# Optimization experiments

Hardware: AMD Instinct MI355X
Metric: run time of the kernel (lower is better)

## Reference

```python
import jax, jax.numpy as jnp
import numpy as np

B, C, H = 128, 3, 224
PATCH_NUM, PS = 14, 16          # patch_size = image_size / patch_num
NP = PATCH_NUM * PATCH_NUM      # 196 patches
TOP_K = 20
D = 768                         # ViT-B hidden dim
NUM_CLASSES = 1000


def setup_inputs() -> dict:
    key = jax.random.key(0)
    k1, k2, k3, k4, k5 = jax.random.split(key, 5)
    return {
        "inputs": jax.random.normal(k1, (B, C, H, H), jnp.float32),
        "patch_grad": jax.random.normal(k2, (B, NP, D), jnp.float32),
        "attack_w": jax.random.uniform(k3, (C, H, H), jnp.float32),  # torch.rand init
        "w_cls": jax.random.normal(k4, (C * NP, NUM_CLASSES), jnp.float32) * 0.02,
        "targets": jax.random.randint(k5, (B,), 0, NUM_CLASSES),
    }


def reference(inputs, patch_grad, attack_w, w_cls, targets):
    # --- top-k patch selection from patch-embedding gradients ---
    # sum over batch, then over embedding dim -> [NP]
    sum_patch = patch_grad.sum(axis=0).sum(axis=1)
    _, top_idx = jax.lax.top_k(sum_patch, TOP_K)  # distinct patch indices

    # --- vectorized equivalent of the per-pixel double loop ---
    # patch (ix, iy) -> pixel block [ix*PS:(ix+1)*PS, iy*PS:(iy+1)*PS]
    ix = top_idx // PATCH_NUM
    iy = top_idx % PATCH_NUM
    mask_p = jnp.zeros((PATCH_NUM, PATCH_NUM), inputs.dtype).at[ix, iy].set(1.0)
    mask = jnp.kron(mask_p, jnp.ones((PS, PS), inputs.dtype))  # [H, H] pixel mask
    x = inputs + mask[None, None, :, :] * attack_w[None, :, :, :]  # [B,C,H,H]

    # --- surrogate classifier head (stand-in for aux_vit second forward) ---
    # per-patch average pool, flatten, linear -> logits [B, NUM_CLASSES]
    pooled = x.reshape(B, C, PATCH_NUM, PS, PATCH_NUM, PS).mean(axis=(3, 5))
    logits = pooled.reshape(B, -1) @ w_cls

    targets_prob = jax.nn.softmax(logits, axis=1)
    # original applies CrossEntropyLoss to the *probabilities* (treats them as logits)
    logp = jax.nn.log_softmax(targets_prob, axis=1)
    ce = -jnp.take_along_axis(logp, targets[:, None], axis=1)[:, 0]  # [B]

    u = 0.0
    l2loss = jnp.mean(attack_w * attack_w)
    loss = u * l2loss - (1.0 - u) * ce.mean()
    return targets_prob, loss
```

## Files before the change

kernel.cpp:

```cpp
#include <hip/hip_runtime.h>
#include <math.h>

#define PA_OFF    0
#define APOOL_OFF 1024
#define MA_OFF    2048
#define IPOOL_OFF 4096
#define PL_OFF    81920

__global__ __launch_bounds__(256) void k1_fused(
    const float* __restrict__ inputs,
    const float* __restrict__ patch_grad,
    const float* __restrict__ attack_w,
    float* __restrict__ ws)
{
  __shared__ __align__(16) float lds[3136];
  const int bid = blockIdx.x;
  const int t   = threadIdx.x;

  if (bid < 384) {
    const int b = bid / 3, c = bid - b * 3;
    const float* img = inputs + (size_t)bid * 50176;
    if (t < 224) {
      const int c4 = t % 56, rg = t / 56;
      for (int px = 0; px < 14; ++px) {
        float s = 0.f;
        #pragma unroll
        for (int jj = 0; jj < 4; ++jj) {
          const int row = px * 16 + jj * 4 + rg;
          const float4 v = *(const float4*)(img + row * 224 + c4 * 4);
          s += v.x + v.y + v.z + v.w;
        }
        lds[(px * 4 + rg) * 56 + c4] = s;
      }
    }
    __syncthreads();
    if (t < 196) {
      const int px = t / 14, py = t - px * 14;
      float s = 0.f;
      #pragma unroll
      for (int rg = 0; rg < 4; ++rg)
        #pragma unroll
        for (int i4 = 0; i4 < 4; ++i4)
          s += lds[(px * 4 + rg) * 56 + py * 4 + i4];
      ws[IPOOL_OFF + (size_t)b * 588 + c * 196 + t] = s * (1.f / 256.f);
    }
  } else if (bid < 1168) {
    const int a = bid - 384;
    const int p = a >> 2, chunk = a & 3;
    const float* base = patch_grad + (size_t)chunk * 32 * 150528 + (size_t)p * 768;
    float ax = 0, ay = 0, az = 0, aw = 0;
    #pragma unroll
    for (int j = 0; j < 24; ++j) {
      const int idx = j * 256 + t;
      const int r   = idx / 192;
      const int off = idx - r * 192;
      const float4 v = *(const float4*)(base + (size_t)r * 150528 + off * 4);
      ax += v.x; ay += v.y; az += v.z; aw += v.w;
    }
    float acc = (ax + ay) + (az + aw);
    #pragma unroll
    for (int o = 32; o > 0; o >>= 1) acc += __shfl_down(acc, o, 64);
    if ((t & 63) == 0) lds[t >> 6] = acc;
    __syncthreads();
    if (t == 0) ws[PA_OFF + a] = lds[0] + lds[1] + lds[2] + lds[3];
  } else {
    const int a = bid - 1168;
    const int c = a / 14, px = a - c * 14;
    const float* img = attack_w + (size_t)c * 50176;
    if (t < 224) {
      const int c4 = t % 56, rg = t / 56;
      float s = 0.f;
      #pragma unroll
      for (int jj = 0; jj < 4; ++jj) {
        const int row = px * 16 + jj * 4 + rg;
        const float4 v = *(const float4*)(img + row * 224 + c4 * 4);
        s += v.x + v.y + v.z + v.w;
      }
      lds[rg * 56 + c4] = s;
    }
    __syncthreads();
    if (t < 14) {
      float s = 0.f;
      #pragma unroll
      for (int rg = 0; rg < 4; ++rg)
        for (int i4 = 0; i4 < 4; ++i4)
          s += lds[rg * 56 + t * 4 + i4];
      ws[APOOL_OFF + c * 196 + px * 14 + t] = s * (1.f / 256.f);
    }
  }
}

__global__ __launch_bounds__(256) void k2_topk(float* __restrict__ ws,
                                               float* __restrict__ d_loss)
{
  __shared__ float sp[196];
  __shared__ float maskp[196];
  const int t = threadIdx.x;
  if (t < 196) {
    const float* pa = ws + PA_OFF;
    float s = 0.f;
    #pragma unroll
    for (int j = 0; j < 4; ++j) s += pa[t * 4 + j];
    sp[t] = s;
  }
  if (t == 0) *d_loss = 0.f;
  __syncthreads();
  if (t < 196) {
    const float v = sp[t];
    int cnt = 0;
    for (int j = 0; j < 196; ++j) {
      const float u = sp[j];
      cnt += (u > v || (u == v && j < t)) ? 1 : 0;
    }
    maskp[t] = (cnt < 20) ? 1.f : 0.f;
  }
  __syncthreads();
  for (int k = t; k < 588; k += 256) {
    const int p = k % 196;
    ws[MA_OFF + k] = maskp[p] * ws[APOOL_OFF + k];
  }
}

__global__ __launch_bounds__(256) void k3_gemm(const float* __restrict__ w_cls,
                                               float* __restrict__ ws)
{
  __shared__ __align__(16) float lp[147 * 16];
  const int bid = blockIdx.x;
  const int ks = bid & 3;
  const int nt = (bid >> 2) & 15;
  const int bg = bid >> 6;
  const int t  = threadIdx.x;
  const float* ipool = ws + IPOOL_OFF;
  const float* ma    = ws + MA_OFF;
  for (int idx = t; idx < 2352; idx += 256) {
    const int bb = idx / 147;
    const int kk = idx - bb * 147;
    const int k  = ks * 147 + kk;
    lp[kk * 16 + bb] = ipool[(size_t)(bg * 16 + bb) * 588 + k] + ma[k];
  }
  __syncthreads();
  const int lane = t & 63, g = t >> 6;
  const int n = nt * 64 + lane;
  const bool valid = n < 1000;
  float a0 = 0, a1 = 0, a2 = 0, a3 = 0;
  const float* wc = w_cls + (size_t)ks * 147 * 1000 + n;
  #pragma unroll 7
  for (int kk = 0; kk < 147; ++kk) {
    const float w = valid ? wc[(size_t)kk * 1000] : 0.f;
    const float4 pv = *(const float4*)&lp[kk * 16 + g * 4];
    a0 += pv.x * w; a1 += pv.y * w; a2 += pv.z * w; a3 += pv.w * w;
  }
  float* pl = ws + PL_OFF;
  const int rowb = ks * 128 + bg * 16 + g * 4;
  pl[(size_t)(rowb + 0) * 1024 + n] = a0;
  pl[(size_t)(rowb + 1) * 1024 + n] = a1;
  pl[(size_t)(rowb + 2) * 1024 + n] = a2;
  pl[(size_t)(rowb + 3) * 1024 + n] = a3;
}

__global__ __launch_bounds__(256) void k4_softmax(const float* __restrict__ ws,
                                                  const int* __restrict__ targets,
                                                  float* __restrict__ out)
{
  __shared__ float red[4];
  __shared__ float sh_pt;
  const int b = blockIdx.x, t = threadIdx.x;
  const float* pl = ws + PL_OFF;
  float l[4]; bool val[4];
  #pragma unroll
  for (int j = 0; j < 4; ++j) {
    const int n = j * 256 + t;
    val[j] = (n < 1000);
    float s = -INFINITY;
    if (val[j]) {
      s = 0.f;
      #pragma unroll
      for (int ks = 0; ks < 4; ++ks) s += pl[(size_t)(ks * 128 + b) * 1024 + n];
    }
    l[j] = s;
  }
  float m = fmaxf(fmaxf(l[0], l[1]), fmaxf(l[2], l[3]));
  #pragma unroll
  for (int o = 32; o > 0; o >>= 1) m = fmaxf(m, __shfl_down(m, o, 64));
  if ((t & 63) == 0) red[t >> 6] = m;
  __syncthreads();
  const float m1 = fmaxf(fmaxf(red[0], red[1]), fmaxf(red[2], red[3]));
  __syncthreads();
  float e[4]; float s = 0.f;
  #pragma unroll
  for (int j = 0; j < 4; ++j) { e[j] = val[j] ? expf(l[j] - m1) : 0.f; s += e[j]; }
  #pragma unroll
  for (int o = 32; o > 0; o >>= 1) s += __shfl_down(s, o, 64);
  if ((t & 63) == 0) red[t >> 6] = s;
  __syncthreads();
  const float S1 = red[0] + red[1] + red[2] + red[3];
  __syncthreads();
  const float inv = 1.f / S1;
  const int tgt = targets[b];
  float p[4];
  #pragma unroll
  for (int j = 0; j < 4; ++j) {
    const int n = j * 256 + t;
    if (val[j]) {
      p[j] = e[j] * inv;
      out[(size_t)b * 1000 + n] = p[j];
      if (n == tgt) sh_pt = p[j];
    } else {
      p[j] = -INFINITY;
    }
  }
  float m2 = fmaxf(fmaxf(p[0], p[1]), fmaxf(p[2], p[3]));
  #pragma unroll
  for (int o = 32; o > 0; o >>= 1) m2 = fmaxf(m2, __shfl_down(m2, o, 64));
  if ((t & 63) == 0) red[t >> 6] = m2;
  __syncthreads();
  const float M2 = fmaxf(fmaxf(red[0], red[1]), fmaxf(red[2], red[3]));
  __syncthreads();
  float s2 = 0.f;
  #pragma unroll
  for (int j = 0; j < 4; ++j) s2 += val[j] ? expf(p[j] - M2) : 0.f;
  #pragma unroll
  for (int o = 32; o > 0; o >>= 1) s2 += __shfl_down(s2, o, 64);
  if ((t & 63) == 0) red[t >> 6] = s2;
  __syncthreads();
  if (t == 0) {
    const float S2 = red[0] + red[1] + red[2] + red[3];
    const float lse2 = M2 + logf(S2);
    atomicAdd(out + 128000, (sh_pt - lse2) * (1.f / 128.f));
  }
}

extern "C" void kernel_launch(void* const* d_in, const int* in_sizes, int n_in,
                              void* d_out, int out_size, void* d_ws, size_t ws_size,
                              hipStream_t stream) {
  const float* inputs     = (const float*)d_in[0];
  const float* patch_grad = (const float*)d_in[1];
  const float* attack_w   = (const float*)d_in[2];
  const float* w_cls      = (const float*)d_in[3];
  const int*   targets    = (const int*)d_in[4];
  float* out = (float*)d_out;
  float* ws  = (float*)d_ws;

  hipLaunchKernelGGL(k1_fused,  dim3(1210), dim3(256), 0, stream,
                     inputs, patch_grad, attack_w, ws);
  hipLaunchKernelGGL(k2_topk,   dim3(1),    dim3(256), 0, stream, ws, out + 128000);
  hipLaunchKernelGGL(k3_gemm,   dim3(512),  dim3(256), 0, stream, w_cls, ws);
  hipLaunchKernelGGL(k4_softmax, dim3(128), dim3(256), 0, stream, ws, targets, out);
}
```

Baseline: 212.2 us.

## Split pooling, patch-grad reduction and GEMM into more, smaller blocks with batched loads

The image-pooling stage is split so each block handles two patch rows of one image channel instead of the whole image. The patch-gradient reduction uses 8 batch chunks instead of 4, and all loads are issued up front into register arrays before summing. The GEMM uses 8-batch groups per block, doubling the block count. The aim is more parallelism and more memory-level parallelism on a bandwidth-bound workload. The cost is more blocks, repeated weight reads in the GEMM, and more partials for the top-k kernel to sum.

```diff
diff --git a/kernel.cpp b/kernel.cpp
--- a/kernel.cpp
+++ b/kernel.cpp
@@ -2,8 +2,8 @@
 #include <math.h>
 
 #define PA_OFF    0
-#define APOOL_OFF 1024
-#define MA_OFF    2048
+#define APOOL_OFF 2048
+#define MA_OFF    3072
 #define IPOOL_OFF 4096
 #define PL_OFF    81920
 
@@ -13,69 +13,77 @@
     const float* __restrict__ attack_w,
     float* __restrict__ ws)
 {
-  __shared__ __align__(16) float lds[3136];
+  __shared__ __align__(16) float lds[448];
   const int bid = blockIdx.x;
   const int t   = threadIdx.x;
 
-  if (bid < 384) {
-    const int b = bid / 3, c = bid - b * 3;
-    const float* img = inputs + (size_t)bid * 50176;
+  if (bid < 2688) {
+    const int img = bid / 7, pp = bid - img * 7;
+    const float* src = inputs + (size_t)img * 50176 + (size_t)pp * 32 * 224;
     if (t < 224) {
       const int c4 = t % 56, rg = t / 56;
-      for (int px = 0; px < 14; ++px) {
-        float s = 0.f;
-        #pragma unroll
-        for (int jj = 0; jj < 4; ++jj) {
-          const int row = px * 16 + jj * 4 + rg;
-          const float4 v = *(const float4*)(img + row * 224 + c4 * 4);
-          s += v.x + v.y + v.z + v.w;
-        }
-        lds[(px * 4 + rg) * 56 + c4] = s;
+      float4 v[8];
+      #pragma unroll
+      for (int j = 0; j < 8; ++j) {
+        const int row = (j >> 2) * 16 + (j & 3) * 4 + rg;
+        v[j] = *(const float4*)(src + row * 224 + c4 * 4);
       }
+      float s0 = 0.f, s1 = 0.f;
+      #pragma unroll
+      for (int j = 0; j < 4; ++j) s0 += (v[j].x + v[j].y) + (v[j].z + v[j].w);
+      #pragma unroll
+      for (int j = 4; j < 8; ++j) s1 += (v[j].x + v[j].y) + (v[j].z + v[j].w);
+      lds[(0 * 4 + rg) * 56 + c4] = s0;
+      lds[(1 * 4 + rg) * 56 + c4] = s1;
     }
     __syncthreads();
-    if (t < 196) {
-      const int px = t / 14, py = t - px * 14;
+    if (t < 28) {
+      const int pxl = t / 14, py = t - pxl * 14;
       float s = 0.f;
       #pragma unroll
       for (int rg = 0; rg < 4; ++rg)
         #pragma unroll
         for (int i4 = 0; i4 < 4; ++i4)
-          s += lds[(px * 4 + rg) * 56 + py * 4 + i4];
-      ws[IPOOL_OFF + (size_t)b * 588 + c * 196 + t] = s * (1.f / 256.f);
-    }
-  } else if (bid < 1168) {
-    const int a = bid - 384;
-    const int p = a >> 2, chunk = a & 3;
-    const float* base = patch_grad + (size_t)chunk * 32 * 150528 + (size_t)p * 768;
-    float ax = 0, ay = 0, az = 0, aw = 0;
-    #pragma unroll
-    for (int j = 0; j < 24; ++j) {
+          s += lds[(pxl * 4 + rg) * 56 + py * 4 + i4];
+      const int b = img / 3, c = img - b * 3;
+      const int px = pp * 2 + pxl;
+      ws[IPOOL_OFF + (size_t)b * 588 + c * 196 + px * 14 + py] = s * (1.f / 256.f);
+    }
+  } else if (bid < 4256) {
+    const int a = bid - 2688;
+    const int p = a >> 3, chunk = a & 7;
+    const float* base = patch_grad + (size_t)chunk * 16 * 150528 + (size_t)p * 768;
+    float4 v[12];
+    #pragma unroll
+    for (int j = 0; j < 12; ++j) {
       const int idx = j * 256 + t;
       const int r   = idx / 192;
       const int off = idx - r * 192;
-      const float4 v = *(const float4*)(base + (size_t)r * 150528 + off * 4);
-      ax += v.x; ay += v.y; az += v.z; aw += v.w;
-    }
-    float acc = (ax + ay) + (az + aw);
+      v[j] = *(const float4*)(base + (size_t)r * 150528 + off * 4);
+    }
+    float acc = 0.f;
+    #pragma unroll
+    for (int j = 0; j < 12; ++j) acc += (v[j].x + v[j].y) + (v[j].z + v[j].w);
     #pragma unroll
     for (int o = 32; o > 0; o >>= 1) acc += __shfl_down(acc, o, 64);
     if ((t & 63) == 0) lds[t >> 6] = acc;
     __syncthreads();
     if (t == 0) ws[PA_OFF + a] = lds[0] + lds[1] + lds[2] + lds[3];
   } else {
-    const int a = bid - 1168;
+    const int a = bid - 4256;
     const int c = a / 14, px = a - c * 14;
     const float* img = attack_w + (size_t)c * 50176;
     if (t < 224) {
       const int c4 = t % 56, rg = t / 56;
-      float s = 0.f;
+      float4 v[4];
       #pragma unroll
       for (int jj = 0; jj < 4; ++jj) {
         const int row = px * 16 + jj * 4 + rg;
-        const float4 v = *(const float4*)(img + row * 224 + c4 * 4);
-        s += v.x + v.y + v.z + v.w;
+        v[jj] = *(const float4*)(img + row * 224 + c4 * 4);
       }
+      float s = 0.f;
+      #pragma unroll
+      for (int jj = 0; jj < 4; ++jj) s += (v[jj].x + v[jj].y) + (v[jj].z + v[jj].w);
       lds[rg * 56 + c4] = s;
     }
     __syncthreads();
@@ -100,7 +108,7 @@
     const float* pa = ws + PA_OFF;
     float s = 0.f;
     #pragma unroll
-    for (int j = 0; j < 4; ++j) s += pa[t * 4 + j];
+    for (int j = 0; j < 8; ++j) s += pa[t * 8 + j];
     sp[t] = s;
   }
   if (t == 0) *d_loss = 0.f;
@@ -124,7 +132,7 @@
 __global__ __launch_bounds__(256) void k3_gemm(const float* __restrict__ w_cls,
                                                float* __restrict__ ws)
 {
-  __shared__ __align__(16) float lp[147 * 16];
+  __shared__ __align__(16) float lp[147 * 8];
   const int bid = blockIdx.x;
   const int ks = bid & 3;
   const int nt = (bid >> 2) & 15;
@@ -132,30 +140,28 @@
   const int t  = threadIdx.x;
   const float* ipool = ws + IPOOL_OFF;
   const float* ma    = ws + MA_OFF;
-  for (int idx = t; idx < 2352; idx += 256) {
+  for (int idx = t; idx < 1176; idx += 256) {
     const int bb = idx / 147;
     const int kk = idx - bb * 147;
     const int k  = ks * 147 + kk;
-    lp[kk * 16 + bb] = ipool[(size_t)(bg * 16 + bb) * 588 + k] + ma[k];
+    lp[kk * 8 + bb] = ipool[(size_t)(bg * 8 + bb) * 588 + k] + ma[k];
   }
   __syncthreads();
   const int lane = t & 63, g = t >> 6;
   const int n = nt * 64 + lane;
   const bool valid = n < 1000;
-  float a0 = 0, a1 = 0, a2 = 0, a3 = 0;
+  float a0 = 0, a1 = 0;
   const float* wc = w_cls + (size_t)ks * 147 * 1000 + n;
   #pragma unroll 7
   for (int kk = 0; kk < 147; ++kk) {
     const float w = valid ? wc[(size_t)kk * 1000] : 0.f;
-    const float4 pv = *(const float4*)&lp[kk * 16 + g * 4];
-    a0 += pv.x * w; a1 += pv.y * w; a2 += pv.z * w; a3 += pv.w * w;
+    const float2 pv = *(const float2*)&lp[kk * 8 + g * 2];
+    a0 += pv.x * w; a1 += pv.y * w;
   }
   float* pl = ws + PL_OFF;
-  const int rowb = ks * 128 + bg * 16 + g * 4;
+  const int rowb = ks * 128 + bg * 8 + g * 2;
   pl[(size_t)(rowb + 0) * 1024 + n] = a0;
   pl[(size_t)(rowb + 1) * 1024 + n] = a1;
-  pl[(size_t)(rowb + 2) * 1024 + n] = a2;
-  pl[(size_t)(rowb + 3) * 1024 + n] = a3;
 }
 
 __global__ __launch_bounds__(256) void k4_softmax(const float* __restrict__ ws,
@@ -241,9 +247,9 @@
   float* out = (float*)d_out;
   float* ws  = (float*)d_ws;
 
-  hipLaunchKernelGGL(k1_fused,  dim3(1210), dim3(256), 0, stream,
+  hipLaunchKernelGGL(k1_fused,  dim3(4298), dim3(256), 0, stream,
                      inputs, patch_grad, attack_w, ws);
   hipLaunchKernelGGL(k2_topk,   dim3(1),    dim3(256), 0, stream, ws, out + 128000);
-  hipLaunchKernelGGL(k3_gemm,   dim3(512),  dim3(256), 0, stream, w_cls, ws);
+  hipLaunchKernelGGL(k3_gemm,   dim3(1024), dim3(256), 0, stream, w_cls, ws);
   hipLaunchKernelGGL(k4_softmax, dim3(128), dim3(256), 0, stream, ws, targets, out);
 }
```

Measured after the change: 207.1 us. 1.02x faster.
